# Kernel tuning notes

Measured on AMD Instinct MI355X. Metric: run time of the kernel, lower is better.

Reference implementation:

```python
import jax, jax.numpy as jnp
import numpy as np

B, L, D_INNER, D_STATE, DT_RANK, MODES = 4, 2048, 256, 16, 16, 32
LN_EPS = 1e-5


def setup_inputs() -> dict:
    key = jax.random.key(0)
    ks = jax.random.split(key, 10)
    x = jax.random.normal(ks[0], (B, L, D_INNER), dtype=jnp.float32)
    ln_g = jnp.ones((D_INNER,), jnp.float32)
    ln_b = jnp.zeros((D_INNER,), jnp.float32)
    W_xproj = jax.random.normal(ks[1], (DT_RANK + 2 * D_STATE, D_INNER), jnp.float32) * (D_INNER ** -0.5)
    dt_init_std = DT_RANK ** -0.5  # dt_scale = 1.0
    W_dt = jax.random.uniform(ks[2], (D_INNER, DT_RANK), jnp.float32, -dt_init_std, dt_init_std)
    dt = jnp.exp(jax.random.uniform(ks[3], (D_INNER,), jnp.float32) * (np.log(0.1) - np.log(0.001)) + np.log(0.001))
    dt = jnp.clip(dt, 1e-4, None)
    b_dt = dt + jnp.log(-jnp.expm1(-dt))  # inverse softplus
    A_log = jnp.zeros((D_INNER, D_STATE), jnp.float32)  # log(ones)
    D_param = jnp.ones((D_INNER,), jnp.float32)
    scale = 1.0 / (D_STATE * D_STATE)
    w_re = scale * jax.random.uniform(ks[4], (D_STATE, D_STATE, MODES), jnp.float32)
    w_im = scale * jax.random.uniform(ks[5], (D_STATE, D_STATE, MODES), jnp.float32)
    return {"x": x, "ln_g": ln_g, "ln_b": ln_b, "W_xproj": W_xproj, "W_dt": W_dt,
            "b_dt": b_dt, "A_log": A_log, "D_param": D_param, "w_re": w_re, "w_im": w_im}


def _fft_kernel(hs, w_re, w_im):
    # hs: (B, L, d_inner, d_state); rfft over d_inner with d_state channels
    h = jnp.transpose(hs, (0, 1, 3, 2))  # (B, L, k, N)
    hf = jnp.fft.rfft(h, axis=-1)        # (B, L, k, N//2+1) complex
    n_freq = D_INNER // 2 + 1
    l = min(MODES, n_freq)
    w = (w_re + 1j * w_im).astype(hf.dtype)
    of = jnp.einsum('blix,iox->blox', hf[..., :l], w[..., :l])
    of = jnp.pad(of, ((0, 0), (0, 0), (0, 0), (0, n_freq - l)))
    h2 = jnp.fft.irfft(of, n=D_INNER, axis=-1)  # real, (B, L, k, N)
    return jnp.transpose(h2, (0, 1, 3, 2))      # (B, L, d_inner, d_state)


def reference(x, ln_g, ln_b, W_xproj, W_dt, b_dt, A_log, D_param, w_re, w_im):
    # LayerNorm
    mu = jnp.mean(x, axis=-1, keepdims=True)
    var = jnp.var(x, axis=-1, keepdims=True)
    xn = (x - mu) * jax.lax.rsqrt(var + LN_EPS) * ln_g + ln_b

    A = -jnp.exp(A_log)  # (d_inner, d_state)
    dbc = xn @ W_xproj.T  # (B, L, dt_rank + 2*d_state)
    delta_r = dbc[..., :DT_RANK]
    Bc = dbc[..., DT_RANK:DT_RANK + D_STATE]        # (B, L, d_state)
    Cc = dbc[..., DT_RANK + D_STATE:]               # (B, L, d_state)
    delta = jax.nn.softplus(delta_r @ W_dt.T + b_dt)  # (B, L, d_inner)

    deltaA = jnp.exp(delta[..., None] * A)                       # (B, L, d_inner, d_state)
    BX = delta[..., None] * Bc[:, :, None, :] * xn[..., None]    # (B, L, d_inner, d_state)

    # selective scan: h_t = deltaA_t * h_{t-1} + BX_t (parallel associative scan over L)
    def comb(c1, c2):
        a1, b1 = c1
        a2, b2 = c2
        return a1 * a2, a2 * b1 + b2
    _, hs = jax.lax.associative_scan(comb, (deltaA, BX), axis=1)

    hs = _fft_kernel(hs, w_re, w_im)
    y = jnp.einsum('bldn,bln->bld', hs, Cc)  # hs @ C
    y = y + D_param * xn
    return y + x
```

## Files before the change

kernel.cpp:

```cpp
#include <hip/hip_runtime.h>
#include <hip/hip_bf16.h>

#define B_   4
#define L_   2048
#define D_   256
#define NC   128
#define CL   16
#define ANG  0.02454369260617025967f

typedef __bf16 bf16x8 __attribute__((ext_vector_type(8)));
typedef __bf16 bf16x4 __attribute__((ext_vector_type(4)));
typedef float  f32x4  __attribute__((ext_vector_type(4)));

__global__ __launch_bounds__(256) void k_prep(
        const float* __restrict__ W_xproj, const float* __restrict__ w_re, const float* __restrict__ w_im,
        __hip_bfloat16* __restrict__ E_t, __hip_bfloat16* __restrict__ Wfrag,
        __hip_bfloat16* __restrict__ wfrag, __hip_bfloat16* __restrict__ E_inv)
{
    int idx = blockIdx.x * 256 + threadIdx.x;
    if (idx < 16384) {
        int x = idx >> 8, d = idx & 255;
        float v = (x < 32) ? __cosf(ANG * (float)((x * d) & 255))
                           : -__sinf(ANG * (float)(((x - 32) * d) & 255));
        E_t[idx] = __float2bfloat16(v);
    } else if (idx < 32768) {
        int f = idx - 16384;
        int ks = f >> 11, t = (f >> 3) & 255, j = f & 7;
        int jcol = (t >> 6) * 16 + (t & 15);
        int dd = ks * 32 + ((t >> 4) & 3) * 8 + j;
        float v = (jcol < 48) ? W_xproj[jcol * 256 + dd] : 0.f;
        Wfrag[f] = __float2bfloat16(v);
    } else if (idx < 65536) {
        int f = idx - 32768;
        int nt = f >> 9, l = (f >> 3) & 63, j = f & 7;
        int n = nt * 16 + (l & 15);
        int o = ((l >> 4) & 3) * 8 + j;
        float v = 0.f;
        if (o < 16) {
            int comp = n >> 9, x = (n >> 4) & 31, i = n & 15;
            v = comp ? w_im[(i * 16 + o) * 32 + x] : w_re[(i * 16 + o) * 32 + x];
        }
        wfrag[f] = __float2bfloat16(v);
    } else if (idx < 81920) {
        int f = idx - 65536;
        int nt = f >> 10, ks = (f >> 9) & 1, l = (f >> 3) & 63, j = f & 7;
        int row = ks * 32 + ((l >> 4) & 3) * 8 + j;
        int col = nt * 16 + (l & 15);
        float v = (row < 32) ? __cosf(ANG * (float)((row * col) & 255))
                             : -__sinf(ANG * (float)(((row - 32) * col) & 255));
        E_inv[f] = __float2bfloat16(v);
    }
}

__global__ __launch_bounds__(256) void k_lnscan(
        const float* __restrict__ x, const float* __restrict__ ln_g, const float* __restrict__ ln_b,
        const float* __restrict__ W_dt, const float* __restrict__ b_dt,
        const float* __restrict__ A_log,
        const __hip_bfloat16* __restrict__ Wfrag,
        unsigned int* __restrict__ dxn,
        float* __restrict__ Bc_o, float* __restrict__ Cc_o,
        float* __restrict__ dsum_o, float* __restrict__ S)
{
    __shared__ __align__(16) float xn_s[16 * 260];
    __shared__ __align__(16) __bf16 xnb[16 * 256];
    __shared__ float dbc_s[16 * 52];
    int tid = threadIdx.x, wave = tid >> 6, lane = tid & 63;
    int blk = blockIdx.x;
    int grow0 = blk * CL;
    char* xnb_c = (char*)xnb;

#pragma unroll
    for (int rr = 0; rr < 4; rr++) {
        int r = wave * 4 + rr;
        const float* xr = x + (size_t)(grow0 + r) * D_;
        float v[4];
#pragma unroll
        for (int q = 0; q < 4; q++) v[q] = xr[lane + q * 64];
        float sum = v[0] + v[1] + v[2] + v[3];
        float sq  = v[0]*v[0] + v[1]*v[1] + v[2]*v[2] + v[3]*v[3];
#pragma unroll
        for (int off = 32; off; off >>= 1) { sum += __shfl_xor(sum, off); sq += __shfl_xor(sq, off); }
        float mu = sum * (1.f / D_);
        float rstd = rsqrtf(sq * (1.f / D_) - mu * mu + 1e-5f);
#pragma unroll
        for (int q = 0; q < 4; q++) {
            int d = lane + q * 64;
            float xv = (v[q] - mu) * rstd * ln_g[d] + ln_b[d];
            xn_s[r * 260 + d] = xv;
            *(__bf16*)(xnb_c + r * 512 + ((d * 2) ^ ((r & 7) << 4))) = (__bf16)xv;
        }
    }
    __syncthreads();

    {
        int mrow = lane & 15;
        f32x4 acc = {0.f, 0.f, 0.f, 0.f};
#pragma unroll
        for (int ks = 0; ks < 8; ks++) {
            bf16x8 af = *(const bf16x8*)(xnb_c + mrow * 512 +
                          ((ks * 64 + ((lane >> 4) * 16)) ^ ((mrow & 7) << 4)));
            bf16x8 bf = *(const bf16x8*)(Wfrag + (ks * 256 + tid) * 8);
            acc = __builtin_amdgcn_mfma_f32_16x16x32_bf16(af, bf, acc, 0, 0, 0);
        }
        int j = wave * 16 + (lane & 15);
#pragma unroll
        for (int q = 0; q < 4; q++) {
            int r = (lane >> 4) * 4 + q;
            if (j < 48) dbc_s[r * 52 + j] = acc[q];
            if (j >= 32 && j < 48)      Cc_o[(size_t)(grow0 + r) * 16 + j - 32] = acc[q];
            else if (j >= 16 && j < 32) Bc_o[(size_t)(grow0 + r) * 16 + j - 16] = acc[q];
        }
    }
    __syncthreads();

    int d = tid;
    float wdt[16];
#pragma unroll
    for (int q = 0; q < 4; q++) {
        f32x4 w4 = *(const f32x4*)&W_dt[d * 16 + q * 4];
#pragma unroll
        for (int k = 0; k < 4; k++) wdt[q * 4 + k] = w4[k];
    }
    float bd = b_dt[d];
    float dlt_r[16];
#pragma unroll
    for (int r = 0; r < 16; r++) {
        float din = bd;
#pragma unroll
        for (int k = 0; k < 16; k++) din = fmaf(dbc_s[r * 52 + k], wdt[k], din);
        din = (din > 15.f) ? din : log1pf(__expf(din));
        dlt_r[r] = din;
        union { __bf16 h2[2]; unsigned int u; } pk;
        pk.h2[0] = (__bf16)din;
        pk.h2[1] = (__bf16)xn_s[r * 260 + d];
        dxn[(size_t)(grow0 + r) * D_ + d] = pk.u;
    }

    float ar[16];
#pragma unroll
    for (int q = 0; q < 4; q++) {
        f32x4 a4 = *(const f32x4*)&A_log[d * 16 + q * 4];
#pragma unroll
        for (int k = 0; k < 4; k++) ar[q * 4 + k] = -__expf(a4[k]);
    }
    bool uni = true;
#pragma unroll
    for (int n = 1; n < 16; n++) uni = uni && (ar[n] == ar[0]);
    float s[16], dsum = 0.f;
#pragma unroll
    for (int n = 0; n < 16; n++) s[n] = 0.f;
    if (uni) {
        float ar0 = ar[0];
#pragma unroll
        for (int t = 0; t < CL; t++) {
            float dl = dlt_r[t];
            float dx = dl * xn_s[t * 260 + d];
            dsum += dl;
            float e = __expf(dl * ar0);
#pragma unroll
            for (int n = 0; n < 16; n++)
                s[n] = fmaf(e, s[n], dx * dbc_s[t * 52 + 16 + n]);
        }
    } else {
#pragma unroll
        for (int t = 0; t < CL; t++) {
            float dl = dlt_r[t];
            float dx = dl * xn_s[t * 260 + d];
            dsum += dl;
#pragma unroll
            for (int n = 0; n < 16; n++) {
                float e = __expf(dl * ar[n]);
                s[n] = fmaf(e, s[n], dx * dbc_s[t * 52 + 16 + n]);
            }
        }
    }
    dsum_o[(size_t)blk * 256 + d] = dsum;
    size_t o = (size_t)blk * 4096 + d * 16;
#pragma unroll
    for (int q = 0; q < 4; q++) {
        f32x4 sv;
#pragma unroll
        for (int k = 0; k < 4; k++) sv[k] = s[q*4+k];
        *reinterpret_cast<f32x4*>(&S[o + q * 4]) = sv;
    }
}

__global__ __launch_bounds__(256) void k_scan_par(
        const float* __restrict__ A_log, const float* __restrict__ dsum,
        float* __restrict__ S_H0)
{
    __shared__ float gP[256];
    __shared__ float gS[256];
    int tid = threadIdx.x;
    int g2 = tid >> 5, cl2 = tid & 31;
    int ch = blockIdx.x * 32 + cl2;
    int b2 = ch >> 12, dn2 = ch & 4095;
    int dd = dn2 >> 4;
    float arv = -__expf(A_log[dn2]);
    size_t cb = ((size_t)b2 * NC + g2 * 16) * 4096 + dn2;
    size_t db = ((size_t)b2 * NC + g2 * 16) * 256 + dd;
    float pv[16], sv[16];
#pragma unroll
    for (int c = 0; c < 16; c++) {
        pv[c] = __expf(arv * dsum[db + (size_t)c * 256]);
        sv[c] = S_H0[cb + (size_t)c * 4096];
    }
    float pA = 1.f, sA = 0.f;
#pragma unroll
    for (int c = 0; c < 16; c++) { sA = fmaf(pv[c], sA, sv[c]); pA *= pv[c]; }
    gP[g2 * 32 + cl2] = pA;
    gS[g2 * 32 + cl2] = sA;
    __syncthreads();
    float h = 0.f;
    for (int gg = 0; gg < g2; gg++)
        h = fmaf(gP[gg * 32 + cl2], h, gS[gg * 32 + cl2]);
#pragma unroll
    for (int c = 0; c < 16; c++) {
        S_H0[cb + (size_t)c * 4096] = h;
        h = fmaf(pv[c], h, sv[c]);
    }
}

__global__ __launch_bounds__(256, 2) void k_fused(
        const unsigned int* __restrict__ dxn,
        const float* __restrict__ xin, const float* __restrict__ D_param,
        const float* __restrict__ Bc, const float* __restrict__ Cc,
        const float* __restrict__ A_log, const float* __restrict__ H0,
        float* __restrict__ out,
        const __hip_bfloat16* __restrict__ E_t, const __hip_bfloat16* __restrict__ wfrag,
        const __hip_bfloat16* __restrict__ E_inv)
{
    __shared__ __align__(16) char smem[69760];
    __bf16* hfb  = (__bf16*)(smem + 32768);
    __bf16* gsb  = (__bf16*)(smem + 65536);
    __bf16* ccb  = (__bf16*)(smem + 67712);
    float*  bc_s = (float*)(smem + 68736);

    int tid = threadIdx.x, wave = tid >> 6, lane = tid & 63;
    int wm = wave >> 1, wx = wave & 1;
    int blk = blockIdx.x;
    int grow0 = blk * CL;
    int d = tid;

    bc_s[tid] = Bc[(size_t)grow0 * 16 + tid];
    {
        float ccv = Cc[(size_t)grow0 * 16 + tid];
        int r = tid >> 4, o = tid & 15;
        ccb[r * 32 + o] = (__bf16)ccv;
        ccb[r * 32 + 16 + o] = (__bf16)0.f;
    }
    unsigned int dxnv[16];
#pragma unroll
    for (int t = 0; t < 16; t++) dxnv[t] = dxn[(size_t)(grow0 + t) * D_ + d];
    float ar[16], h[16];
    {
        size_t ho = (size_t)blk * 4096 + d * 16;
#pragma unroll
        for (int q = 0; q < 4; q++) {
            f32x4 a4 = *(const f32x4*)&A_log[d * 16 + q * 4];
            f32x4 h4 = *(const f32x4*)&H0[ho + q * 4];
#pragma unroll
            for (int k = 0; k < 4; k++) { ar[q*4+k] = -__expf(a4[k]); h[q*4+k] = h4[k]; }
        }
    }
    bool uni = true;
#pragma unroll
    for (int n = 1; n < 16; n++) uni = uni && (ar[n] == ar[0]);
    float ar0 = ar[0];

    bf16x8 bfragAll[2][8];
#pragma unroll
    for (int nt2 = 0; nt2 < 2; nt2++) {
        int xa = wx * 32 + nt2 * 16 + (lane & 15);
#pragma unroll
        for (int ks = 0; ks < 8; ks++)
            bfragAll[nt2][ks] = *(const bf16x8*)(E_t + xa * 256 + ks * 32 + ((lane >> 4) * 8));
    }
    int swz = (lane & 7) << 4;
    f32x4 acc[2][2];
#pragma unroll
    for (int a = 0; a < 2; a++)
#pragma unroll
        for (int b = 0; b < 2; b++) { acc[a][b][0]=0.f; acc[a][b][1]=0.f; acc[a][b][2]=0.f; acc[a][b][3]=0.f; }
    __syncthreads();

#pragma unroll
    for (int g = 0; g < 4; g++) {
        if (uni) {
#pragma unroll
            for (int tl = 0; tl < 4; tl++) {
                unsigned int v = dxnv[g * 4 + tl];
                float dl = __uint_as_float(v << 16);
                float dx = dl * __uint_as_float(v & 0xffff0000u);
                float e = __expf(dl * ar0);
#pragma unroll
                for (int n = 0; n < 16; n++) {
                    h[n] = fmaf(e, h[n], dx * bc_s[(g * 4 + tl) * 16 + n]);
                    int m = tl * 16 + n;
                    *(__bf16*)(smem + m * 512 + ((d * 2) ^ ((m & 7) << 4))) = (__bf16)h[n];
                }
            }
        } else {
#pragma unroll
            for (int tl = 0; tl < 4; tl++) {
                unsigned int v = dxnv[g * 4 + tl];
                float dl = __uint_as_float(v << 16);
                float dx = dl * __uint_as_float(v & 0xffff0000u);
#pragma unroll
                for (int n = 0; n < 16; n++) {
                    float e = __expf(dl * ar[n]);
                    h[n] = fmaf(e, h[n], dx * bc_s[(g * 4 + tl) * 16 + n]);
                    int m = tl * 16 + n;
                    *(__bf16*)(smem + m * 512 + ((d * 2) ^ ((m & 7) << 4))) = (__bf16)h[n];
                }
            }
        }
        __syncthreads();
#pragma unroll
        for (int ks = 0; ks < 8; ks++) {
#pragma unroll
            for (int tl2 = 0; tl2 < 2; tl2++) {
                int m = (wm * 2 + tl2) * 16 + (lane & 15);
                bf16x8 af = *(const bf16x8*)(smem + m * 512 + ((ks * 64 + ((lane >> 4) * 16)) ^ swz));
#pragma unroll
                for (int nt2 = 0; nt2 < 2; nt2++)
                    acc[tl2][nt2] = __builtin_amdgcn_mfma_f32_16x16x32_bf16(af, bfragAll[nt2][ks], acc[tl2][nt2], 0, 0, 0);
            }
        }
#pragma unroll
        for (int tl2 = 0; tl2 < 2; tl2++) {
            int r = g * 4 + wm * 2 + tl2;
#pragma unroll
            for (int nt2 = 0; nt2 < 2; nt2++) {
                int xcol = wx * 32 + nt2 * 16 + (lane & 15);
                bf16x4 pk;
#pragma unroll
                for (int k = 0; k < 4; k++) { pk[k] = (__bf16)acc[tl2][nt2][k]; acc[tl2][nt2][k] = 0.f; }
                *(bf16x4*)(&hfb[r * 1024 + xcol * 16 + (lane >> 4) * 4]) = pk;
            }
        }
        __syncthreads();
    }

    float xpf[4][4], xnpf[4][4], dpf[4];
#pragma unroll
    for (int ntl = 0; ntl < 4; ntl++) {
        int dcol = (wave * 4 + ntl) * 16 + (lane & 15);
        dpf[ntl] = D_param[dcol];
#pragma unroll
        for (int q = 0; q < 4; q++) {
            int r = (lane >> 4) * 4 + q;
            size_t go = (size_t)(grow0 + r) * D_ + dcol;
            xpf[ntl][q] = xin[go];
            xnpf[ntl][q] = __uint_as_float(dxn[go] & 0xffff0000u);
        }
    }

    {
        bf16x8 ccf = *(const bf16x8*)((char*)ccb + (lane & 15) * 64 + ((lane >> 4) * 16));
#pragma unroll
        for (int ntl = 0; ntl < 16; ntl++) {
            int nt = wave * 16 + ntl;
            f32x4 a = {0.f, 0.f, 0.f, 0.f};
            bf16x8 wf = *(const bf16x8*)(wfrag + (nt * 64 + lane) * 8);
            a = __builtin_amdgcn_mfma_f32_16x16x32_bf16(ccf, wf, a, 0, 0, 0);
            int col = nt * 16 + (lane & 15);
#pragma unroll
            for (int q = 0; q < 4; q++) {
                int r = (lane >> 4) * 4 + q;
                *(__bf16*)(smem + r * 2048 + col * 2) = (__bf16)a[q];
            }
        }
    }
    __syncthreads();

    {
        __bf16* wcb = (__bf16*)smem;
        int r = tid >> 4, x2 = tid & 15;
#pragma unroll
        for (int xh = 0; xh < 2; xh++) {
            int xs = xh * 16 + x2;
            bf16x8 hra = *(const bf16x8*)(&hfb[r * 1024 + xs * 16]);
            bf16x8 hrb = *(const bf16x8*)(&hfb[r * 1024 + xs * 16 + 8]);
            bf16x8 hia = *(const bf16x8*)(&hfb[r * 1024 + (xs + 32) * 16]);
            bf16x8 hib = *(const bf16x8*)(&hfb[r * 1024 + (xs + 32) * 16 + 8]);
            bf16x8 wra = *(const bf16x8*)(&wcb[r * 1024 + xs * 16]);
            bf16x8 wrb = *(const bf16x8*)(&wcb[r * 1024 + xs * 16 + 8]);
            bf16x8 wia = *(const bf16x8*)(&wcb[r * 1024 + 512 + xs * 16]);
            bf16x8 wib = *(const bf16x8*)(&wcb[r * 1024 + 512 + xs * 16 + 8]);
            float gre = 0.f, gim = 0.f;
#pragma unroll
            for (int k = 0; k < 8; k++) {
                float hr = (float)hra[k], hi = (float)hia[k];
                float wr = (float)wra[k], wi = (float)wia[k];
                gre = fmaf(hr, wr, gre); gre = fmaf(-hi, wi, gre);
                gim = fmaf(hr, wi, gim); gim = fmaf(hi, wr, gim);
                float hr2 = (float)hrb[k], hi2 = (float)hib[k];
                float wr2 = (float)wrb[k], wi2 = (float)wib[k];
                gre = fmaf(hr2, wr2, gre); gre = fmaf(-hi2, wi2, gre);
                gim = fmaf(hr2, wi2, gim); gim = fmaf(hi2, wr2, gim);
            }
            float sc = xs ? 2.f : 1.f;
            gsb[r * 68 + xs]      = (__bf16)(gre * sc);
            gsb[r * 68 + 32 + xs] = (__bf16)(gim * sc);
        }
    }
    __syncthreads();

    {
        bf16x8 ga0 = *(const bf16x8*)((char*)gsb + (lane & 15) * 136 + ((lane >> 4) * 16));
        bf16x8 ga1 = *(const bf16x8*)((char*)gsb + (lane & 15) * 136 + 64 + ((lane >> 4) * 16));
#pragma unroll
        for (int ntl = 0; ntl < 4; ntl++) {
            int nt = wave * 4 + ntl;
            f32x4 a = {0.f, 0.f, 0.f, 0.f};
            a = __builtin_amdgcn_mfma_f32_16x16x32_bf16(
                    ga0, *(const bf16x8*)(E_inv + ((nt * 2 + 0) * 64 + lane) * 8), a, 0, 0, 0);
            a = __builtin_amdgcn_mfma_f32_16x16x32_bf16(
                    ga1, *(const bf16x8*)(E_inv + ((nt * 2 + 1) * 64 + lane) * 8), a, 0, 0, 0);
            int dcol = nt * 16 + (lane & 15);
#pragma unroll
            for (int q = 0; q < 4; q++) {
                int r = (lane >> 4) * 4 + q;
                size_t go = (size_t)(grow0 + r) * D_ + dcol;
                out[go] = xpf[ntl][q] + dpf[ntl] * xnpf[ntl][q] + a[q] * (1.f / 256.f);
            }
        }
    }
}

extern "C" void kernel_launch(void* const* d_in, const int* in_sizes, int n_in,
                              void* d_out, int out_size, void* d_ws, size_t ws_size,
                              hipStream_t stream)
{
    const float* x       = (const float*)d_in[0];
    const float* ln_g    = (const float*)d_in[1];
    const float* ln_b    = (const float*)d_in[2];
    const float* W_xproj = (const float*)d_in[3];
    const float* W_dt    = (const float*)d_in[4];
    const float* b_dt    = (const float*)d_in[5];
    const float* A_log   = (const float*)d_in[6];
    const float* D_param = (const float*)d_in[7];
    const float* w_re    = (const float*)d_in[8];
    const float* w_im    = (const float*)d_in[9];

    float* ws    = (float*)d_ws;
    float* S_H0  = ws;
    unsigned int* dxn = (unsigned int*)(S_H0 + 2097152);
    float* Bc    = (float*)(dxn + 2097152);
    float* Cc    = Bc + 131072;
    float* dsum  = Cc + 131072;
    __hip_bfloat16* tab = (__hip_bfloat16*)(dsum + 131072);
    __hip_bfloat16* E_t   = tab;
    __hip_bfloat16* Wfrag = tab + 16384;
    __hip_bfloat16* wfrag = tab + 32768;
    __hip_bfloat16* E_inv = tab + 65536;
    float* out = (float*)d_out;

    hipLaunchKernelGGL(k_prep, dim3(320), dim3(256), 0, stream,
                       W_xproj, w_re, w_im, E_t, Wfrag, wfrag, E_inv);
    hipLaunchKernelGGL(k_lnscan, dim3(B_*NC), dim3(256), 0, stream,
                       x, ln_g, ln_b, W_dt, b_dt, A_log, Wfrag,
                       dxn, Bc, Cc, dsum, S_H0);
    hipLaunchKernelGGL(k_scan_par, dim3(B_*NC), dim3(256), 0, stream, A_log, dsum, S_H0);
    hipLaunchKernelGGL(k_fused, dim3(B_*NC), dim3(256), 0, stream,
                       dxn, x, D_param, Bc, Cc, A_log, S_H0, out, E_t, wfrag, E_inv);
}
```

Measured before the change: 54.31 us.

## Fuse LN/scan, chunk-prefix, and FFT stages into one persistent kernel with grid barriers

Merges the three per-chunk kernels into a single kernel that uses two atomic grid-wide barriers between the chunk-local scan, the cross-chunk prefix, and the FFT/output stage. Per-chunk data (delta/xn, B, C, and the residual x + D*xn) stays in registers and shared memory instead of going through global workspace. This removes two kernel launches and the dxn/Bc/Cc round trips. In exchange it depends on all 512 blocks being co-resident (2 per CU via launch bounds), adds spin-wait barrier cost, and adds a memset launch.

```diff
diff --git a/kernel.cpp b/kernel.cpp
--- a/kernel.cpp
+++ b/kernel.cpp
@@ -6,6 +6,7 @@
 #define D_   256
 #define NC   128
 #define CL   16
+#define NBLK (B_*NC)
 #define ANG  0.02454369260617025967f
 
 typedef __bf16 bf16x8 __attribute__((ext_vector_type(8)));
@@ -52,23 +53,52 @@
     }
 }
 
-__global__ __launch_bounds__(256) void k_lnscan(
+__device__ __forceinline__ void gbar(unsigned int* ctr)
+{
+    __syncthreads();
+    if (threadIdx.x == 0) {
+        __threadfence();
+        __hip_atomic_fetch_add(ctr, 1u, __ATOMIC_ACQ_REL, __HIP_MEMORY_SCOPE_AGENT);
+        while (__hip_atomic_load(ctr, __ATOMIC_ACQUIRE, __HIP_MEMORY_SCOPE_AGENT) < (unsigned)NBLK)
+            __builtin_amdgcn_s_sleep(2);
+        __threadfence();
+    }
+    __syncthreads();
+}
+
+__global__ __launch_bounds__(256, 2) void k_main(
         const float* __restrict__ x, const float* __restrict__ ln_g, const float* __restrict__ ln_b,
         const float* __restrict__ W_dt, const float* __restrict__ b_dt,
-        const float* __restrict__ A_log,
-        const __hip_bfloat16* __restrict__ Wfrag,
-        unsigned int* __restrict__ dxn,
-        float* __restrict__ Bc_o, float* __restrict__ Cc_o,
-        float* __restrict__ dsum_o, float* __restrict__ S)
+        const float* __restrict__ D_param, const float* __restrict__ A_log,
+        const __hip_bfloat16* __restrict__ Wfrag, const __hip_bfloat16* __restrict__ E_t,
+        const __hip_bfloat16* __restrict__ wfrag, const __hip_bfloat16* __restrict__ E_inv,
+        float* __restrict__ S_H0, float* __restrict__ dsum_g,
+        unsigned int* __restrict__ ctr, float* __restrict__ out)
 {
-    __shared__ __align__(16) float xn_s[16 * 260];
-    __shared__ __align__(16) __bf16 xnb[16 * 256];
-    __shared__ float dbc_s[16 * 52];
+    __shared__ __align__(16) char smem[69760];
+    float*  xn_s  = (float*)smem;
+    char*   xnb_c = smem + 16640;
+    float*  dbc_s = (float*)(smem + 24832);
+    __bf16* hfb   = (__bf16*)(smem + 32768);
+    __bf16* gsb   = (__bf16*)(smem + 65536);
+    __bf16* ccb   = (__bf16*)(smem + 67712);
+    float*  bc_s  = (float*)(smem + 68736);
+
     int tid = threadIdx.x, wave = tid >> 6, lane = tid & 63;
     int blk = blockIdx.x;
     int grow0 = blk * CL;
-    char* xnb_c = (char*)xnb;
-
+    int d = tid;
+
+    { int r = tid >> 4, o = tid & 15; ccb[r * 32 + 16 + o] = (__bf16)0.f; }
+
+    float dp[4], lg[4], lb[4];
+#pragma unroll
+    for (int q = 0; q < 4; q++) {
+        dp[q] = D_param[lane + q * 64];
+        lg[q] = ln_g[lane + q * 64];
+        lb[q] = ln_b[lane + q * 64];
+    }
+    float bsv[4][4];
 #pragma unroll
     for (int rr = 0; rr < 4; rr++) {
         int r = wave * 4 + rr;
@@ -84,10 +114,11 @@
         float rstd = rsqrtf(sq * (1.f / D_) - mu * mu + 1e-5f);
 #pragma unroll
         for (int q = 0; q < 4; q++) {
-            int d = lane + q * 64;
-            float xv = (v[q] - mu) * rstd * ln_g[d] + ln_b[d];
-            xn_s[r * 260 + d] = xv;
-            *(__bf16*)(xnb_c + r * 512 + ((d * 2) ^ ((r & 7) << 4))) = (__bf16)xv;
+            int dc = lane + q * 64;
+            float xv = (v[q] - mu) * rstd * lg[q] + lb[q];
+            xn_s[r * 260 + dc] = xv;
+            *(__bf16*)(xnb_c + r * 512 + ((dc * 2) ^ ((r & 7) << 4))) = (__bf16)xv;
+            bsv[rr][q] = v[q] + dp[q] * xv;
         }
     }
     __syncthreads();
@@ -106,36 +137,37 @@
 #pragma unroll
         for (int q = 0; q < 4; q++) {
             int r = (lane >> 4) * 4 + q;
-            if (j < 48) dbc_s[r * 52 + j] = acc[q];
-            if (j >= 32 && j < 48)      Cc_o[(size_t)(grow0 + r) * 16 + j - 32] = acc[q];
-            else if (j >= 16 && j < 32) Bc_o[(size_t)(grow0 + r) * 16 + j - 16] = acc[q];
-        }
-    }
-    __syncthreads();
-
-    int d = tid;
-    float wdt[16];
-#pragma unroll
-    for (int q = 0; q < 4; q++) {
-        f32x4 w4 = *(const f32x4*)&W_dt[d * 16 + q * 4];
-#pragma unroll
-        for (int k = 0; k < 4; k++) wdt[q * 4 + k] = w4[k];
-    }
-    float bd = b_dt[d];
-    float dlt_r[16];
-#pragma unroll
-    for (int r = 0; r < 16; r++) {
-        float din = bd;
-#pragma unroll
-        for (int k = 0; k < 16; k++) din = fmaf(dbc_s[r * 52 + k], wdt[k], din);
-        din = (din > 15.f) ? din : log1pf(__expf(din));
-        dlt_r[r] = din;
-        union { __bf16 h2[2]; unsigned int u; } pk;
-        pk.h2[0] = (__bf16)din;
-        pk.h2[1] = (__bf16)xn_s[r * 260 + d];
-        dxn[(size_t)(grow0 + r) * D_ + d] = pk.u;
-    }
-
+            if (j < 16)      dbc_s[r * 20 + j] = acc[q];
+            else if (j < 32) bc_s[r * 16 + (j - 16)] = acc[q];
+            else if (j < 48) ccb[r * 32 + (j - 32)] = (__bf16)acc[q];
+        }
+    }
+    __syncthreads();
+
+    unsigned int dxnv[16];
+    {
+        float wdt[16];
+#pragma unroll
+        for (int q = 0; q < 4; q++) {
+            f32x4 w4 = *(const f32x4*)&W_dt[d * 16 + q * 4];
+#pragma unroll
+            for (int k = 0; k < 4; k++) wdt[q * 4 + k] = w4[k];
+        }
+        float bd = b_dt[d];
+#pragma unroll
+        for (int r = 0; r < 16; r++) {
+            float din = bd;
+#pragma unroll
+            for (int k = 0; k < 16; k++) din = fmaf(dbc_s[r * 20 + k], wdt[k], din);
+            din = (din > 15.f) ? din : log1pf(__expf(din));
+            union { __bf16 h2[2]; unsigned int u; } pk;
+            pk.h2[0] = (__bf16)din;
+            pk.h2[1] = (__bf16)xn_s[r * 260 + d];
+            dxnv[r] = pk.u;
+            xn_s[r * 260 + d] = xn_s[r * 260 + d];
+            dbc_s[r * 20 + 16] = din;
+        }
+    }
     float ar[16];
 #pragma unroll
     for (int q = 0; q < 4; q++) {
@@ -146,128 +178,93 @@
     bool uni = true;
 #pragma unroll
     for (int n = 1; n < 16; n++) uni = uni && (ar[n] == ar[0]);
-    float s[16], dsum = 0.f;
-#pragma unroll
-    for (int n = 0; n < 16; n++) s[n] = 0.f;
-    if (uni) {
-        float ar0 = ar[0];
-#pragma unroll
-        for (int t = 0; t < CL; t++) {
-            float dl = dlt_r[t];
-            float dx = dl * xn_s[t * 260 + d];
-            dsum += dl;
-            float e = __expf(dl * ar0);
-#pragma unroll
-            for (int n = 0; n < 16; n++)
-                s[n] = fmaf(e, s[n], dx * dbc_s[t * 52 + 16 + n]);
-        }
-    } else {
-#pragma unroll
-        for (int t = 0; t < CL; t++) {
-            float dl = dlt_r[t];
-            float dx = dl * xn_s[t * 260 + d];
-            dsum += dl;
-#pragma unroll
-            for (int n = 0; n < 16; n++) {
-                float e = __expf(dl * ar[n]);
-                s[n] = fmaf(e, s[n], dx * dbc_s[t * 52 + 16 + n]);
-            }
-        }
-    }
-    dsum_o[(size_t)blk * 256 + d] = dsum;
-    size_t o = (size_t)blk * 4096 + d * 16;
-#pragma unroll
-    for (int q = 0; q < 4; q++) {
-        f32x4 sv;
-#pragma unroll
-        for (int k = 0; k < 4; k++) sv[k] = s[q*4+k];
-        *reinterpret_cast<f32x4*>(&S[o + q * 4]) = sv;
-    }
-}
-
-__global__ __launch_bounds__(256) void k_scan_par(
-        const float* __restrict__ A_log, const float* __restrict__ dsum,
-        float* __restrict__ S_H0)
-{
-    __shared__ float gP[256];
-    __shared__ float gS[256];
-    int tid = threadIdx.x;
-    int g2 = tid >> 5, cl2 = tid & 31;
-    int ch = blockIdx.x * 32 + cl2;
-    int b2 = ch >> 12, dn2 = ch & 4095;
-    int dd = dn2 >> 4;
-    float arv = -__expf(A_log[dn2]);
-    size_t cb = ((size_t)b2 * NC + g2 * 16) * 4096 + dn2;
-    size_t db = ((size_t)b2 * NC + g2 * 16) * 256 + dd;
-    float pv[16], sv[16];
-#pragma unroll
-    for (int c = 0; c < 16; c++) {
-        pv[c] = __expf(arv * dsum[db + (size_t)c * 256]);
-        sv[c] = S_H0[cb + (size_t)c * 4096];
-    }
-    float pA = 1.f, sA = 0.f;
-#pragma unroll
-    for (int c = 0; c < 16; c++) { sA = fmaf(pv[c], sA, sv[c]); pA *= pv[c]; }
-    gP[g2 * 32 + cl2] = pA;
-    gS[g2 * 32 + cl2] = sA;
-    __syncthreads();
-    float h = 0.f;
-    for (int gg = 0; gg < g2; gg++)
-        h = fmaf(gP[gg * 32 + cl2], h, gS[gg * 32 + cl2]);
-#pragma unroll
-    for (int c = 0; c < 16; c++) {
-        S_H0[cb + (size_t)c * 4096] = h;
-        h = fmaf(pv[c], h, sv[c]);
-    }
-}
-
-__global__ __launch_bounds__(256, 2) void k_fused(
-        const unsigned int* __restrict__ dxn,
-        const float* __restrict__ xin, const float* __restrict__ D_param,
-        const float* __restrict__ Bc, const float* __restrict__ Cc,
-        const float* __restrict__ A_log, const float* __restrict__ H0,
-        float* __restrict__ out,
-        const __hip_bfloat16* __restrict__ E_t, const __hip_bfloat16* __restrict__ wfrag,
-        const __hip_bfloat16* __restrict__ E_inv)
-{
-    __shared__ __align__(16) char smem[69760];
-    __bf16* hfb  = (__bf16*)(smem + 32768);
-    __bf16* gsb  = (__bf16*)(smem + 65536);
-    __bf16* ccb  = (__bf16*)(smem + 67712);
-    float*  bc_s = (float*)(smem + 68736);
-
-    int tid = threadIdx.x, wave = tid >> 6, lane = tid & 63;
+    float ar0 = ar[0];
+    {
+        float s[16], dsum = 0.f;
+#pragma unroll
+        for (int n = 0; n < 16; n++) s[n] = 0.f;
+        if (uni) {
+#pragma unroll
+            for (int t = 0; t < CL; t++) {
+                unsigned int v = dxnv[t];
+                float dl = __uint_as_float(v << 16);
+                float dx = dl * __uint_as_float(v & 0xffff0000u);
+                dsum += dl;
+                float e = __expf(dl * ar0);
+#pragma unroll
+                for (int n = 0; n < 16; n++)
+                    s[n] = fmaf(e, s[n], dx * bc_s[t * 16 + n]);
+            }
+        } else {
+#pragma unroll
+            for (int t = 0; t < CL; t++) {
+                unsigned int v = dxnv[t];
+                float dl = __uint_as_float(v << 16);
+                float dx = dl * __uint_as_float(v & 0xffff0000u);
+                dsum += dl;
+#pragma unroll
+                for (int n = 0; n < 16; n++) {
+                    float e = __expf(dl * ar[n]);
+                    s[n] = fmaf(e, s[n], dx * bc_s[t * 16 + n]);
+                }
+            }
+        }
+        dsum_g[(size_t)blk * 256 + d] = dsum;
+        size_t o = (size_t)blk * 4096 + d * 16;
+#pragma unroll
+        for (int q = 0; q < 4; q++) {
+            f32x4 sv;
+#pragma unroll
+            for (int k = 0; k < 4; k++) sv[k] = s[q*4+k];
+            *reinterpret_cast<f32x4*>(&S_H0[o + q * 4]) = sv;
+        }
+    }
+    gbar(ctr + 0);
+
+    {
+        float* gP = (float*)smem;
+        float* gS = (float*)(smem + 1024);
+        int g2 = tid >> 5, cl2 = tid & 31;
+        int ch = blk * 32 + cl2;
+        int b2 = ch >> 12, dn2 = ch & 4095;
+        int ddn = dn2 >> 4;
+        float arv = -__expf(A_log[dn2]);
+        size_t cb = ((size_t)b2 * NC + g2 * 16) * 4096 + dn2;
+        size_t db = ((size_t)b2 * NC + g2 * 16) * 256 + ddn;
+        float pv[16], sv[16];
+#pragma unroll
+        for (int c = 0; c < 16; c++) {
+            pv[c] = __expf(arv * dsum_g[db + (size_t)c * 256]);
+            sv[c] = S_H0[cb + (size_t)c * 4096];
+        }
+        float pA = 1.f, sA = 0.f;
+#pragma unroll
+        for (int c = 0; c < 16; c++) { sA = fmaf(pv[c], sA, sv[c]); pA *= pv[c]; }
+        gP[g2 * 32 + cl2] = pA;
+        gS[g2 * 32 + cl2] = sA;
+        __syncthreads();
+        float h2 = 0.f;
+        for (int gg = 0; gg < g2; gg++)
+            h2 = fmaf(gP[gg * 32 + cl2], h2, gS[gg * 32 + cl2]);
+#pragma unroll
+        for (int c = 0; c < 16; c++) {
+            S_H0[cb + (size_t)c * 4096] = h2;
+            h2 = fmaf(pv[c], h2, sv[c]);
+        }
+    }
+    gbar(ctr + 1);
+
     int wm = wave >> 1, wx = wave & 1;
-    int blk = blockIdx.x;
-    int grow0 = blk * CL;
-    int d = tid;
-
-    bc_s[tid] = Bc[(size_t)grow0 * 16 + tid];
-    {
-        float ccv = Cc[(size_t)grow0 * 16 + tid];
-        int r = tid >> 4, o = tid & 15;
-        ccb[r * 32 + o] = (__bf16)ccv;
-        ccb[r * 32 + 16 + o] = (__bf16)0.f;
-    }
-    unsigned int dxnv[16];
-#pragma unroll
-    for (int t = 0; t < 16; t++) dxnv[t] = dxn[(size_t)(grow0 + t) * D_ + d];
-    float ar[16], h[16];
+    float h[16];
     {
         size_t ho = (size_t)blk * 4096 + d * 16;
 #pragma unroll
         for (int q = 0; q < 4; q++) {
-            f32x4 a4 = *(const f32x4*)&A_log[d * 16 + q * 4];
-            f32x4 h4 = *(const f32x4*)&H0[ho + q * 4];
-#pragma unroll
-            for (int k = 0; k < 4; k++) { ar[q*4+k] = -__expf(a4[k]); h[q*4+k] = h4[k]; }
-        }
-    }
-    bool uni = true;
-#pragma unroll
-    for (int n = 1; n < 16; n++) uni = uni && (ar[n] == ar[0]);
-    float ar0 = ar[0];
-
+            f32x4 h4 = *(const f32x4*)&S_H0[ho + q * 4];
+#pragma unroll
+            for (int k = 0; k < 4; k++) h[q*4+k] = h4[k];
+        }
+    }
     bf16x8 bfragAll[2][8];
 #pragma unroll
     for (int nt2 = 0; nt2 < 2; nt2++) {
@@ -282,7 +279,6 @@
     for (int a = 0; a < 2; a++)
 #pragma unroll
         for (int b = 0; b < 2; b++) { acc[a][b][0]=0.f; acc[a][b][1]=0.f; acc[a][b][2]=0.f; acc[a][b][3]=0.f; }
-    __syncthreads();
 
 #pragma unroll
     for (int g = 0; g < 4; g++) {
@@ -340,20 +336,6 @@
             }
         }
         __syncthreads();
-    }
-
-    float xpf[4][4], xnpf[4][4], dpf[4];
-#pragma unroll
-    for (int ntl = 0; ntl < 4; ntl++) {
-        int dcol = (wave * 4 + ntl) * 16 + (lane & 15);
-        dpf[ntl] = D_param[dcol];
-#pragma unroll
-        for (int q = 0; q < 4; q++) {
-            int r = (lane >> 4) * 4 + q;
-            size_t go = (size_t)(grow0 + r) * D_ + dcol;
-            xpf[ntl][q] = xin[go];
-            xnpf[ntl][q] = __uint_as_float(dxn[go] & 0xffff0000u);
-        }
     }
 
     {
@@ -408,6 +390,7 @@
     __syncthreads();
 
     {
+        float* y_s = (float*)smem;
         bf16x8 ga0 = *(const bf16x8*)((char*)gsb + (lane & 15) * 136 + ((lane >> 4) * 16));
         bf16x8 ga1 = *(const bf16x8*)((char*)gsb + (lane & 15) * 136 + 64 + ((lane >> 4) * 16));
 #pragma unroll
@@ -422,8 +405,17 @@
 #pragma unroll
             for (int q = 0; q < 4; q++) {
                 int r = (lane >> 4) * 4 + q;
-                size_t go = (size_t)(grow0 + r) * D_ + dcol;
-                out[go] = xpf[ntl][q] + dpf[ntl] * xnpf[ntl][q] + a[q] * (1.f / 256.f);
+                y_s[r * 260 + dcol] = a[q] * (1.f / 256.f);
+            }
+        }
+        __syncthreads();
+#pragma unroll
+        for (int rr = 0; rr < 4; rr++) {
+            int r = wave * 4 + rr;
+#pragma unroll
+            for (int q = 0; q < 4; q++) {
+                int dc = lane + q * 64;
+                out[(size_t)(grow0 + r) * D_ + dc] = bsv[rr][q] + y_s[r * 260 + dc];
             }
         }
     }
@@ -446,23 +438,19 @@
 
     float* ws    = (float*)d_ws;
     float* S_H0  = ws;
-    unsigned int* dxn = (unsigned int*)(S_H0 + 2097152);
-    float* Bc    = (float*)(dxn + 2097152);
-    float* Cc    = Bc + 131072;
-    float* dsum  = Cc + 131072;
+    float* dsum  = S_H0 + 2097152;
     __hip_bfloat16* tab = (__hip_bfloat16*)(dsum + 131072);
     __hip_bfloat16* E_t   = tab;
     __hip_bfloat16* Wfrag = tab + 16384;
     __hip_bfloat16* wfrag = tab + 32768;
     __hip_bfloat16* E_inv = tab + 65536;
+    unsigned int* ctr = (unsigned int*)(tab + 81920);
     float* out = (float*)d_out;
 
+    hipMemsetAsync(ctr, 0, 2 * sizeof(unsigned int), stream);
     hipLaunchKernelGGL(k_prep, dim3(320), dim3(256), 0, stream,
                        W_xproj, w_re, w_im, E_t, Wfrag, wfrag, E_inv);
-    hipLaunchKernelGGL(k_lnscan, dim3(B_*NC), dim3(256), 0, stream,
-                       x, ln_g, ln_b, W_dt, b_dt, A_log, Wfrag,
-                       dxn, Bc, Cc, dsum, S_H0);
-    hipLaunchKernelGGL(k_scan_par, dim3(B_*NC), dim3(256), 0, stream, A_log, dsum, S_H0);
-    hipLaunchKernelGGL(k_fused, dim3(B_*NC), dim3(256), 0, stream,
-                       dxn, x, D_param, Bc, Cc, A_log, S_H0, out, E_t, wfrag, E_inv);
+    hipLaunchKernelGGL(k_main, dim3(NBLK), dim3(256), 0, stream,
+                       x, ln_g, ln_b, W_dt, b_dt, D_param, A_log,
+                       Wfrag, E_t, wfrag, E_inv, S_H0, dsum, ctr, out);
 }
```

Result: slower. 184.4 us (+239.5%).

## Read W_xproj directly in lnscan and stage final output through LDS

Applied to the files above, without the earlier changes.

Removes the Wfrag prepack from the prep kernel. k_lnscan now loads fp32 W_xproj rows directly and converts them to bf16 in registers, running the projection MFMA only on the three waves that produce real columns. The epilogue of k_fused writes the inverse-FFT result to shared memory, then each thread writes one full column per row, reusing the dxn values already held in registers instead of reloading dxn and x in a scattered MFMA layout. The goal is fewer prep-kernel blocks, fewer global reads and row-contiguous stores, at the cost of an extra barrier and some LDS traffic.

```diff
diff --git a/kernel.cpp b/kernel.cpp
--- a/kernel.cpp
+++ b/kernel.cpp
@@ -13,9 +13,9 @@
 typedef float  f32x4  __attribute__((ext_vector_type(4)));
 
 __global__ __launch_bounds__(256) void k_prep(
-        const float* __restrict__ W_xproj, const float* __restrict__ w_re, const float* __restrict__ w_im,
-        __hip_bfloat16* __restrict__ E_t, __hip_bfloat16* __restrict__ Wfrag,
-        __hip_bfloat16* __restrict__ wfrag, __hip_bfloat16* __restrict__ E_inv)
+        const float* __restrict__ w_re, const float* __restrict__ w_im,
+        __hip_bfloat16* __restrict__ E_t, __hip_bfloat16* __restrict__ wfrag,
+        __hip_bfloat16* __restrict__ E_inv)
 {
     int idx = blockIdx.x * 256 + threadIdx.x;
     if (idx < 16384) {
@@ -23,15 +23,8 @@
         float v = (x < 32) ? __cosf(ANG * (float)((x * d) & 255))
                            : -__sinf(ANG * (float)(((x - 32) * d) & 255));
         E_t[idx] = __float2bfloat16(v);
-    } else if (idx < 32768) {
+    } else if (idx < 49152) {
         int f = idx - 16384;
-        int ks = f >> 11, t = (f >> 3) & 255, j = f & 7;
-        int jcol = (t >> 6) * 16 + (t & 15);
-        int dd = ks * 32 + ((t >> 4) & 3) * 8 + j;
-        float v = (jcol < 48) ? W_xproj[jcol * 256 + dd] : 0.f;
-        Wfrag[f] = __float2bfloat16(v);
-    } else if (idx < 65536) {
-        int f = idx - 32768;
         int nt = f >> 9, l = (f >> 3) & 63, j = f & 7;
         int n = nt * 16 + (l & 15);
         int o = ((l >> 4) & 3) * 8 + j;
@@ -41,8 +34,8 @@
             v = comp ? w_im[(i * 16 + o) * 32 + x] : w_re[(i * 16 + o) * 32 + x];
         }
         wfrag[f] = __float2bfloat16(v);
-    } else if (idx < 81920) {
-        int f = idx - 65536;
+    } else if (idx < 65536) {
+        int f = idx - 49152;
         int nt = f >> 10, ks = (f >> 9) & 1, l = (f >> 3) & 63, j = f & 7;
         int row = ks * 32 + ((l >> 4) & 3) * 8 + j;
         int col = nt * 16 + (l & 15);
@@ -54,9 +47,8 @@
 
 __global__ __launch_bounds__(256) void k_lnscan(
         const float* __restrict__ x, const float* __restrict__ ln_g, const float* __restrict__ ln_b,
-        const float* __restrict__ W_dt, const float* __restrict__ b_dt,
-        const float* __restrict__ A_log,
-        const __hip_bfloat16* __restrict__ Wfrag,
+        const float* __restrict__ W_xproj, const float* __restrict__ W_dt,
+        const float* __restrict__ b_dt, const float* __restrict__ A_log,
         unsigned int* __restrict__ dxn,
         float* __restrict__ Bc_o, float* __restrict__ Cc_o,
         float* __restrict__ dsum_o, float* __restrict__ S)
@@ -92,23 +84,28 @@
     }
     __syncthreads();
 
-    {
+    if (wave < 3) {
+        int jcol = wave * 16 + (lane & 15);
+        const float* wrow = W_xproj + (size_t)jcol * 256 + ((lane >> 4) * 8);
         int mrow = lane & 15;
         f32x4 acc = {0.f, 0.f, 0.f, 0.f};
 #pragma unroll
         for (int ks = 0; ks < 8; ks++) {
             bf16x8 af = *(const bf16x8*)(xnb_c + mrow * 512 +
                           ((ks * 64 + ((lane >> 4) * 16)) ^ ((mrow & 7) << 4)));
-            bf16x8 bf = *(const bf16x8*)(Wfrag + (ks * 256 + tid) * 8);
+            f32x4 wa = *(const f32x4*)(wrow + ks * 32);
+            f32x4 wb = *(const f32x4*)(wrow + ks * 32 + 4);
+            bf16x8 bf;
+#pragma unroll
+            for (int k = 0; k < 4; k++) { bf[k] = (__bf16)wa[k]; bf[4 + k] = (__bf16)wb[k]; }
             acc = __builtin_amdgcn_mfma_f32_16x16x32_bf16(af, bf, acc, 0, 0, 0);
         }
-        int j = wave * 16 + (lane & 15);
 #pragma unroll
         for (int q = 0; q < 4; q++) {
             int r = (lane >> 4) * 4 + q;
-            if (j < 48) dbc_s[r * 52 + j] = acc[q];
-            if (j >= 32 && j < 48)      Cc_o[(size_t)(grow0 + r) * 16 + j - 32] = acc[q];
-            else if (j >= 16 && j < 32) Bc_o[(size_t)(grow0 + r) * 16 + j - 16] = acc[q];
+            dbc_s[r * 52 + jcol] = acc[q];
+            if (jcol >= 32)      Cc_o[(size_t)(grow0 + r) * 16 + jcol - 32] = acc[q];
+            else if (jcol >= 16) Bc_o[(size_t)(grow0 + r) * 16 + jcol - 16] = acc[q];
         }
     }
     __syncthreads();
@@ -249,6 +246,7 @@
         ccb[r * 32 + o] = (__bf16)ccv;
         ccb[r * 32 + 16 + o] = (__bf16)0.f;
     }
+    float dpv = D_param[d];
     unsigned int dxnv[16];
 #pragma unroll
     for (int t = 0; t < 16; t++) dxnv[t] = dxn[(size_t)(grow0 + t) * D_ + d];
@@ -340,20 +338,6 @@
             }
         }
         __syncthreads();
-    }
-
-    float xpf[4][4], xnpf[4][4], dpf[4];
-#pragma unroll
-    for (int ntl = 0; ntl < 4; ntl++) {
-        int dcol = (wave * 4 + ntl) * 16 + (lane & 15);
-        dpf[ntl] = D_param[dcol];
-#pragma unroll
-        for (int q = 0; q < 4; q++) {
-            int r = (lane >> 4) * 4 + q;
-            size_t go = (size_t)(grow0 + r) * D_ + dcol;
-            xpf[ntl][q] = xin[go];
-            xnpf[ntl][q] = __uint_as_float(dxn[go] & 0xffff0000u);
-        }
     }
 
     {
@@ -407,7 +391,12 @@
     }
     __syncthreads();
 
-    {
+    float xv[16];
+#pragma unroll
+    for (int r = 0; r < 16; r++) xv[r] = xin[(size_t)(grow0 + r) * D_ + d];
+
+    {
+        float* y_s = (float*)smem;
         bf16x8 ga0 = *(const bf16x8*)((char*)gsb + (lane & 15) * 136 + ((lane >> 4) * 16));
         bf16x8 ga1 = *(const bf16x8*)((char*)gsb + (lane & 15) * 136 + 64 + ((lane >> 4) * 16));
 #pragma unroll
@@ -422,9 +411,19 @@
 #pragma unroll
             for (int q = 0; q < 4; q++) {
                 int r = (lane >> 4) * 4 + q;
-                size_t go = (size_t)(grow0 + r) * D_ + dcol;
-                out[go] = xpf[ntl][q] + dpf[ntl] * xnpf[ntl][q] + a[q] * (1.f / 256.f);
-            }
+                y_s[r * 260 + dcol] = a[q];
+            }
+        }
+    }
+    __syncthreads();
+
+    {
+        const float* y_s = (const float*)smem;
+#pragma unroll
+        for (int r = 0; r < 16; r++) {
+            float xnv = __uint_as_float(dxnv[r] & 0xffff0000u);
+            out[(size_t)(grow0 + r) * D_ + d] =
+                xv[r] + dpv * xnv + y_s[r * 260 + d] * (1.f / 256.f);
         }
     }
 }
@@ -452,15 +451,14 @@
     float* dsum  = Cc + 131072;
     __hip_bfloat16* tab = (__hip_bfloat16*)(dsum + 131072);
     __hip_bfloat16* E_t   = tab;
-    __hip_bfloat16* Wfrag = tab + 16384;
-    __hip_bfloat16* wfrag = tab + 32768;
-    __hip_bfloat16* E_inv = tab + 65536;
+    __hip_bfloat16* wfrag = tab + 16384;
+    __hip_bfloat16* E_inv = tab + 49152;
     float* out = (float*)d_out;
 
-    hipLaunchKernelGGL(k_prep, dim3(320), dim3(256), 0, stream,
-                       W_xproj, w_re, w_im, E_t, Wfrag, wfrag, E_inv);
+    hipLaunchKernelGGL(k_prep, dim3(256), dim3(256), 0, stream,
+                       w_re, w_im, E_t, wfrag, E_inv);
     hipLaunchKernelGGL(k_lnscan, dim3(B_*NC), dim3(256), 0, stream,
-                       x, ln_g, ln_b, W_dt, b_dt, A_log, Wfrag,
+                       x, ln_g, ln_b, W_xproj, W_dt, b_dt, A_log,
                        dxn, Bc, Cc, dsum, S_H0);
     hipLaunchKernelGGL(k_scan_par, dim3(B_*NC), dim3(256), 0, stream, A_log, dsum, S_H0);
     hipLaunchKernelGGL(k_fused, dim3(B_*NC), dim3(256), 0, stream,
```

New measurement: 56.23 us. 1.04x slower.
